# Performance work log

Hardware: AMD Instinct MI355X
Metric: run time of the kernel (lower is better)

Reference implementation:

```python
import jax, jax.numpy as jnp
import numpy as np

B, S, D_IN, D_OUT = 4, 2048, 1024, 1024

def setup_inputs() -> dict:
    key = jax.random.key(0)
    ks = jax.random.split(key, 6)
    s = 1.0 / np.sqrt(D_IN)
    return {
        "inputs": jax.random.normal(ks[0], (B, S, D_IN), dtype=jnp.float32),
        "Wq": jax.random.normal(ks[1], (D_IN, D_OUT), dtype=jnp.float32) * s,
        "Wk": jax.random.normal(ks[2], (D_IN, D_OUT), dtype=jnp.float32) * s,
        "Wv": jax.random.normal(ks[3], (D_IN, D_OUT), dtype=jnp.float32) * s,
        "Wo": jax.random.normal(ks[4], (D_OUT, D_OUT), dtype=jnp.float32) * (1.0 / np.sqrt(D_OUT)),
        "bo": jax.random.normal(ks[5], (D_OUT,), dtype=jnp.float32) * 0.01,
    }

def reference(inputs, Wq, Wk, Wv, Wo, bo):
    # QKV projections (no bias, matching qkv_bias=False)
    q = inputs @ Wq  # [B,S,D]
    k = inputs @ Wk
    v = inputs @ Wv
    # naive full attention: scores [B,S,S]
    scores = jnp.einsum('bqd,bkd->bqk', q, k) / jnp.sqrt(jnp.asarray(k.shape[-1], q.dtype))
    attn = jax.nn.softmax(scores, axis=-1)
    out = jnp.einsum('bqk,bkd->bqd', attn, v)
    return out @ Wo + bo
```

## Files before the change

kernel.cpp:

```cpp
#include <hip/hip_runtime.h>
#include <hip/hip_bf16.h>
#include <cstdint>

typedef __attribute__((ext_vector_type(8))) __bf16 bf16x8;
typedef __attribute__((ext_vector_type(4))) float  f32x4;

__device__ __forceinline__ unsigned short f2bf(float x) {
    union { float f; unsigned u; } v; v.f = x;
    unsigned r = v.u + 0x7fffu + ((v.u >> 16) & 1u);
    return (unsigned short)(r >> 16);
}
__device__ __forceinline__ unsigned pack2bf(float a, float b) {
    return (unsigned)f2bf(a) | ((unsigned)f2bf(b) << 16);
}

__device__ __forceinline__ void gld_lds16(const unsigned short* g, unsigned short* l) {
    __builtin_amdgcn_global_load_lds(
        (const __attribute__((address_space(1))) unsigned int*)g,
        (__attribute__((address_space(3))) unsigned int*)l,
        16, 0, 0);
}

__global__ void cvt_kernel(const float* __restrict__ in, unsigned short* __restrict__ out, int n4) {
    int i = blockIdx.x * blockDim.x + threadIdx.x;
    if (i < n4) {
        float4 f = ((const float4*)in)[i];
        ushort4 o;
        o.x = f2bf(f.x); o.y = f2bf(f.y); o.z = f2bf(f.z); o.w = f2bf(f.w);
        ((ushort4*)out)[i] = o;
    }
}

__global__ void wpack_kernel(const float* __restrict__ W, unsigned short* __restrict__ out) {
    int tid  = threadIdx.x;
    int lane = tid & 63;
    int chunk = blockIdx.x * 4 + (tid >> 6);
    int nt = chunk >> 5, k32 = chunk & 31;
    int r = lane & 15, q = lane >> 4;
    const float* src = W + (size_t)(k32*32 + q*8) * 1024 + nt*16 + r;
    unsigned o[4];
#pragma unroll
    for (int i = 0; i < 4; i++)
        o[i] = pack2bf(src[(size_t)(2*i) * 1024], src[(size_t)(2*i+1) * 1024]);
    *(uint4*)(out + (size_t)chunk * 512 + lane * 8) = make_uint4(o[0], o[1], o[2], o[3]);
}

__global__ void softmax_kernel(unsigned short* __restrict__ S) {
    const size_t row = blockIdx.x;
    unsigned short* p = S + row * 2048;
    const int tid = threadIdx.x;
    const int wave = tid >> 6, lane = tid & 63;

    uint4 raw = ((const uint4*)p)[tid];
    unsigned u[4] = {raw.x, raw.y, raw.z, raw.w};
    float x[8];
#pragma unroll
    for (int i = 0; i < 4; i++) {
        x[2*i]   = __uint_as_float(u[i] << 16);
        x[2*i+1] = __uint_as_float(u[i] & 0xffff0000u);
    }
    float m = x[0];
#pragma unroll
    for (int i = 1; i < 8; i++) m = fmaxf(m, x[i]);
#pragma unroll
    for (int off = 32; off >= 1; off >>= 1) m = fmaxf(m, __shfl_xor(m, off, 64));
    __shared__ float sm[4], ss[4];
    if (lane == 0) sm[wave] = m;
    __syncthreads();
    m = fmaxf(fmaxf(sm[0], sm[1]), fmaxf(sm[2], sm[3]));

    float e[8], s = 0.f;
#pragma unroll
    for (int i = 0; i < 8; i++) { e[i] = __expf(x[i] - m); s += e[i]; }
#pragma unroll
    for (int off = 32; off >= 1; off >>= 1) s += __shfl_xor(s, off, 64);
    if (lane == 0) ss[wave] = s;
    __syncthreads();
    s = ss[0] + ss[1] + ss[2] + ss[3];
    float inv = 1.0f / s;

    unsigned o[4];
#pragma unroll
    for (int i = 0; i < 4; i++)
        o[i] = pack2bf(e[2*i] * inv, e[2*i+1] * inv);
    ((uint4*)p)[tid] = make_uint4(o[0], o[1], o[2], o[3]);
}

template<int EPI>
__global__ __launch_bounds__(512, 2)
void gemm8p(const unsigned short* __restrict__ A, const unsigned short* __restrict__ Bpk,
            void* __restrict__ C, unsigned short* __restrict__ Ck, unsigned short* __restrict__ Cv,
            int lda, int ldc, int KS, int ns, float scale,
            long long sA, long long sB, long long sC)
{
    __shared__ __align__(16) char smem[131072];

    const int tid  = threadIdx.x;
    const int lane = tid & 63;
    const int wave = tid >> 6;
    const int bz = blockIdx.z;
    A   += (size_t)bz * sA;
    Bpk += (size_t)bz * sB;

    const int gx = gridDim.x;
    int lin = blockIdx.y * gx + blockIdx.x;
    int cpx = (gx * gridDim.y) >> 3;
    int swz = (lin & 7) * cpx + (lin >> 3);
    const int bm = (swz / gx) * 256;
    const int bn = (swz % gx) * 256;

    const int wm = (wave & 1) * 128;
    const int wn = (wave >> 1) * 64;
    const int ln15 = lane & 15;
    const int quad = lane >> 4;
    const int fko = (quad ^ ((ln15 >> 1) & 3)) * 8;

    const int srow = tid >> 2;
    const int scol = ((tid & 3) ^ ((tid >> 3) & 3)) * 8;
    const unsigned short* paU = A + (size_t)(bm + srow) * lda + scol;
    const unsigned short* paL = A + (size_t)(bm + 128 + srow) * lda + scol;
    const unsigned short* pb0 = Bpk + (size_t)((bn >> 4) + (tid >> 6)) * KS * 512 + lane * 8;
    const long long pbstep = (long long)8 * KS * 512;

    f32x4 acc[8][4];
#pragma unroll
    for (int i = 0; i < 8; i++)
#pragma unroll
        for (int j = 0; j < 4; j++) acc[i][j] = (f32x4){0.f, 0.f, 0.f, 0.f};

    auto stageA = [&](int buf, int t, int k) {
        char* d = smem + buf * 32768 + k * 16384 + tid * 16;
        const unsigned short* s = paU + t * 64 + k * 32;
        gld_lds16(s, (unsigned short*)d);
        gld_lds16(paL + t * 64 + k * 32, (unsigned short*)(d + 8192));
    };
    auto stageB = [&](int buf, int t, int k) {
        char* d = smem + 65536 + buf * 32768 + k * 16384 + (tid >> 6) * 1024 + lane * 16;
        const unsigned short* s = pb0 + (size_t)(2 * t + k) * 512;
        gld_lds16(s, (unsigned short*)d);
        gld_lds16(s + pbstep, (unsigned short*)(d + 8192));
    };
    auto phase = [&](int buf, int k, int mh) {
        const unsigned short* Ar = (const unsigned short*)(smem + buf * 32768 + k * 16384);
        const unsigned short* Br = (const unsigned short*)(smem + 65536 + buf * 32768 + k * 16384);
        bf16x8 af[4], bf[4];
#pragma unroll
        for (int i = 0; i < 4; i++)
            af[i] = *(const bf16x8*)&Ar[(wm + mh * 64 + i * 16 + ln15) * 32 + fko];
#pragma unroll
        for (int j = 0; j < 4; j++)
            bf[j] = *(const bf16x8*)&Br[((wn >> 4) + j) * 512 + lane * 8];
        __builtin_amdgcn_s_setprio(1);
#pragma unroll
        for (int i = 0; i < 4; i++)
#pragma unroll
            for (int j = 0; j < 4; j++)
                acc[mh * 4 + i][j] = __builtin_amdgcn_mfma_f32_16x16x32_bf16(
                    af[i], bf[j], acc[mh * 4 + i][j], 0, 0, 0);
        __builtin_amdgcn_s_setprio(0);
    };

#define SB  __builtin_amdgcn_sched_barrier(0)
#define FEN asm volatile("" ::: "memory")
    stageB(0, 0, 0); stageA(0, 0, 0); stageB(0, 0, 1); stageA(0, 0, 1); SB;

    for (int t = 0; t < ns; ++t) {
        const int buf = t & 1, nb = buf ^ 1;
        const int tn = (t + 1 < ns) ? t + 1 : 0;
        asm volatile("s_waitcnt vmcnt(4)" ::: "memory");
        __builtin_amdgcn_s_barrier(); FEN;
        stageB(nb, tn, 0); SB;
        phase(buf, 0, 0);
        __builtin_amdgcn_s_barrier(); FEN;
        stageA(nb, tn, 0); SB;
        phase(buf, 0, 1);
        asm volatile("s_waitcnt vmcnt(4)" ::: "memory");
        __builtin_amdgcn_s_barrier(); FEN;
        stageB(nb, tn, 1); SB;
        phase(buf, 1, 0);
        __builtin_amdgcn_s_barrier(); FEN;
        stageA(nb, tn, 1); SB;
        phase(buf, 1, 1);
    }
#undef SB
#undef FEN

    if (EPI == 1) {
        __syncthreads();
        float* ep = (float*)(smem + wave * 4352);
        unsigned short* Co = (unsigned short*)C + (size_t)bz * sC;
#pragma unroll
        for (int i = 0; i < 8; i++) {
#pragma unroll
            for (int j = 0; j < 4; j++)
#pragma unroll
                for (int r = 0; r < 4; r++)
                    ep[(quad*4 + r) * 68 + j*16 + ln15] = acc[i][j][r] * scale;
            __builtin_amdgcn_s_waitcnt(0);
#pragma unroll
            for (int pp = 0; pp < 2; pp++) {
                int lrow = pp*8 + (lane >> 3);
                int col0 = (lane & 7) * 8;
                float4 lo = *(const float4*)&ep[lrow * 68 + col0];
                float4 hi = *(const float4*)&ep[lrow * 68 + col0 + 4];
                uint4 o;
                o.x = pack2bf(lo.x, lo.y); o.y = pack2bf(lo.z, lo.w);
                o.z = pack2bf(hi.x, hi.y); o.w = pack2bf(hi.z, hi.w);
                *(uint4*)&Co[(size_t)(bm + wm + i*16 + lrow) * ldc + bn + wn + col0] = o;
            }
            __builtin_amdgcn_s_waitcnt(0);
        }
    } else {
        __syncthreads();
        float* ep = (float*)(smem + wave * 8704);
        const int region = bn >> 10;
#pragma unroll
        for (int g = 0; g < 4; g++) {
#pragma unroll
            for (int ii = 0; ii < 2; ii++) {
                int i = g*2 + ii;
#pragma unroll
                for (int j = 0; j < 4; j++)
#pragma unroll
                    for (int r = 0; r < 4; r++)
                        ep[(ii*16 + quad*4 + r) * 68 + j*16 + ln15] = acc[i][j][r] * scale;
            }
            __builtin_amdgcn_s_waitcnt(0);
            const int mrow0 = bm + wm + g*32;
            if (region == 0) {
                unsigned short* Q = (unsigned short*)C;
#pragma unroll
                for (int pp = 0; pp < 4; pp++) {
                    int lrow = pp*8 + (lane >> 3);
                    int col0 = (lane & 7) * 8;
                    float4 lo = *(const float4*)&ep[lrow * 68 + col0];
                    float4 hi = *(const float4*)&ep[lrow * 68 + col0 + 4];
                    uint4 o;
                    o.x = pack2bf(lo.x, lo.y); o.y = pack2bf(lo.z, lo.w);
                    o.z = pack2bf(hi.x, hi.y); o.w = pack2bf(hi.z, hi.w);
                    *(uint4*)&Q[(size_t)(mrow0 + lrow) * ldc + bn + wn + col0] = o;
                }
            } else if (region == 1) {
#pragma unroll
                for (int mt = 0; mt < 2; mt++)
#pragma unroll
                    for (int c = 0; c < 2; c++) {
                        float4 f0 = *(const float4*)&ep[(mt*16 + ln15) * 68 + c*32 + quad*8];
                        float4 f1 = *(const float4*)&ep[(mt*16 + ln15) * 68 + c*32 + quad*8 + 4];
                        uint4 o;
                        o.x = pack2bf(f0.x, f0.y); o.y = pack2bf(f0.z, f0.w);
                        o.z = pack2bf(f1.x, f1.y); o.w = pack2bf(f1.z, f1.w);
                        int cid = ((mrow0 + mt*16) >> 4) * 32 + ((bn - 1024 + wn + c*32) >> 5);
                        *(uint4*)(Ck + (size_t)cid * 512 + lane * 8) = o;
                    }
            } else {
                int s32 = mrow0 >> 5;
#pragma unroll
                for (int dt = 0; dt < 4; dt++) {
                    float v[8];
#pragma unroll
                    for (int e = 0; e < 8; e++)
                        v[e] = ep[(quad*8 + e) * 68 + dt*16 + ln15];
                    uint4 o;
                    o.x = pack2bf(v[0], v[1]); o.y = pack2bf(v[2], v[3]);
                    o.z = pack2bf(v[4], v[5]); o.w = pack2bf(v[6], v[7]);
                    int cid = (((bn - 2048 + wn) >> 4) + dt) * 256 + s32;
                    *(uint4*)(Cv + (size_t)cid * 512 + lane * 8) = o;
                }
            }
            __builtin_amdgcn_s_waitcnt(0);
        }
    }
}

template<int EPI>
__global__ __launch_bounds__(512, 2)
void gemm_pk(const unsigned short* __restrict__ A, const unsigned short* __restrict__ Bpk,
             void* __restrict__ C, unsigned short* __restrict__ Ck, unsigned short* __restrict__ Cv,
             const float* __restrict__ bias,
             int lda, int ldc, int KS, int ns, float scale,
             long long sA, long long sB, long long sC)
{
    __shared__ __align__(16) char smem[98304];

    const int tid  = threadIdx.x;
    const int lane = tid & 63;
    const int wave = tid >> 6;
    const int bz = blockIdx.z;
    A   += (size_t)bz * sA;
    Bpk += (size_t)bz * sB;

    const int gx = gridDim.x;
    int lin = blockIdx.y * gx + blockIdx.x;
    int cpx = (gx * gridDim.y) >> 3;
    int swz = (lin & 7) * cpx + (lin >> 3);
    const int bm = (swz / gx) * 256;
    const int bn = (swz % gx) * 128;

    const int srow = tid >> 2;
    const int scol = ((tid & 3) ^ ((tid >> 3) & 3)) * 8;
    const unsigned short* pa0 = A + (size_t)(bm + srow) * lda + scol;
    const unsigned short* pa1 = pa0 + 32;
    const unsigned short* pa2 = A + (size_t)(bm + 128 + srow) * lda + scol;
    const unsigned short* pa3 = pa2 + 32;

    const int wm = (wave & 3) * 64;
    const int wn = (wave >> 2) * 64;
    const int ln15 = lane & 15;
    const int quad = lane >> 4;
    const int fko = (quad ^ ((ln15 >> 1) & 3)) * 8;
    const int rbase = (wm >> 7) * 4096 + (wm & 127) * 32;
    const int ldsoff = tid * 16;

    const unsigned short* pb[4];
#pragma unroll
    for (int j = 0; j < 4; j++)
        pb[j] = Bpk + (size_t)(((bn + wn + j*16) >> 4) * KS) * 512 + lane * 8;

    f32x4 acc[4][4];
#pragma unroll
    for (int i = 0; i < 4; i++)
#pragma unroll
        for (int j = 0; j < 4; j++) acc[i][j] = (f32x4){0.f, 0.f, 0.f, 0.f};

    auto dma = [&](int buf) {
        char* base = smem + buf * 32768;
        gld_lds16(pa0, (unsigned short*)(base + ldsoff));
        gld_lds16(pa2, (unsigned short*)(base + 8192  + ldsoff));
        gld_lds16(pa1, (unsigned short*)(base + 16384 + ldsoff));
        gld_lds16(pa3, (unsigned short*)(base + 24576 + ldsoff));
        pa0 += 64; pa1 += 64; pa2 += 64; pa3 += 64;
    };
    auto loadB = [&](bf16x8* br) {
#pragma unroll
        for (int j = 0; j < 4; j++) {
            br[j]     = *(const bf16x8*)(pb[j]);
            br[4 + j] = *(const bf16x8*)(pb[j] + 512);
            pb[j] += 1024;
        }
    };
    auto phase = [&](const unsigned short* As, int t, const bf16x8* br) {
        bf16x8 af[4];
#pragma unroll
        for (int i = 0; i < 4; i++)
            af[i] = *(const bf16x8*)&As[t*8192 + rbase + i*512 + ln15*32 + fko];
        __builtin_amdgcn_s_setprio(1);
#pragma unroll
        for (int i = 0; i < 4; i++)
#pragma unroll
            for (int j = 0; j < 4; j++)
                acc[i][j] = __builtin_amdgcn_mfma_f32_16x16x32_bf16(
                    af[i], br[t*4 + j], acc[i][j], 0, 0, 0);
        __builtin_amdgcn_s_setprio(0);
    };

#define SB __builtin_amdgcn_sched_barrier(0)
    bf16x8 b0[8], b1[8];
    SB; dma(0); SB; loadB(b0); SB; dma(1); SB;

    int p = 0;
    for (int it = 0; it < ns; it += 2) {
        const unsigned short* As0 = (const unsigned short*)(smem + p * 32768);
        int p1 = p + 1; if (p1 >= 3) p1 -= 3;
        int q0 = p + 2; if (q0 >= 3) q0 -= 3;
        const unsigned short* As1 = (const unsigned short*)(smem + p1 * 32768);
        const bool more = (it + 2 < ns);

        asm volatile("s_waitcnt vmcnt(12)" ::: "memory");
        SB; __builtin_amdgcn_s_barrier(); SB;
        loadB(b1); SB;
        phase(As0, 0, b0);
        __builtin_amdgcn_s_barrier(); SB;
        if (more) { dma(q0); SB; }
        phase(As0, 1, b0);

        if (more) { asm volatile("s_waitcnt vmcnt(12)" ::: "memory"); }
        else      { asm volatile("s_waitcnt vmcnt(8)"  ::: "memory"); }
        SB; __builtin_amdgcn_s_barrier(); SB;
        if (more) { loadB(b0); SB; }
        phase(As1, 0, b1);
        __builtin_amdgcn_s_barrier(); SB;
        if (it + 3 < ns) { dma(p); SB; }
        phase(As1, 1, b1);

        p = q0;
    }
#undef SB

    if (EPI == 0) {
        float bval[4];
#pragma unroll
        for (int j = 0; j < 4; j++) bval[j] = bias[bn + wn + j*16 + ln15];
        float* Co = (float*)C + (size_t)bz * sC;
#pragma unroll
        for (int i = 0; i < 4; i++) {
            int r0 = bm + wm + i*16 + quad*4;
#pragma unroll
            for (int j = 0; j < 4; j++) {
                int c = bn + wn + j*16 + ln15;
#pragma unroll
                for (int r = 0; r < 4; r++)
                    Co[(size_t)(r0 + r) * ldc + c] = acc[i][j][r] * scale + bval[j];
            }
        }
    } else if (EPI == 1) {
        __syncthreads();
        float* ep = (float*)(smem + wave * 4352);
        unsigned short* Co = (unsigned short*)C + (size_t)bz * sC;
#pragma unroll
        for (int i = 0; i < 4; i++) {
#pragma unroll
            for (int j = 0; j < 4; j++)
#pragma unroll
                for (int r = 0; r < 4; r++)
                    ep[(quad*4 + r) * 68 + j*16 + ln15] = acc[i][j][r] * scale;
            __builtin_amdgcn_s_waitcnt(0);
#pragma unroll
            for (int pp = 0; pp < 2; pp++) {
                int lrow = pp*8 + (lane >> 3);
                int col0 = (lane & 7) * 8;
                float4 lo = *(const float4*)&ep[lrow * 68 + col0];
                float4 hi = *(const float4*)&ep[lrow * 68 + col0 + 4];
                uint4 o;
                o.x = pack2bf(lo.x, lo.y); o.y = pack2bf(lo.z, lo.w);
                o.z = pack2bf(hi.x, hi.y); o.w = pack2bf(hi.z, hi.w);
                *(uint4*)&Co[(size_t)(bm + wm + i*16 + lrow) * ldc + bn + wn + col0] = o;
            }
            __builtin_amdgcn_s_waitcnt(0);
        }
    }
}

extern "C" void kernel_launch(void* const* d_in, const int* in_sizes, int n_in,
                              void* d_out, int out_size, void* d_ws, size_t ws_size,
                              hipStream_t stream) {
    const float* X  = (const float*)d_in[0];
    const float* Wq = (const float*)d_in[1];
    const float* Wk = (const float*)d_in[2];
    const float* Wv = (const float*)d_in[3];
    const float* Wo = (const float*)d_in[4];
    const float* bo = (const float*)d_in[5];
    float* out = (float*)d_out;

    size_t off = 0;
    auto alloc = [&](size_t bytes) {
        void* p = (char*)d_ws + off;
        off += (bytes + 255) & ~(size_t)255;
        return p;
    };
    unsigned short* Xbf  = (unsigned short*)alloc(8192ull * 1024 * 2);
    unsigned short* Wpk  = (unsigned short*)alloc(192ull * 32 * 512 * 2);
    unsigned short* Wopk = (unsigned short*)alloc(64ull * 32 * 512 * 2);
    unsigned short* Qrm  = (unsigned short*)alloc(8192ull * 1024 * 2);
    unsigned short* Kpk  = (unsigned short*)alloc(512ull * 32 * 512 * 2);
    unsigned short* Vpk  = (unsigned short*)alloc(64ull * 256 * 512 * 2);
    unsigned short* Sc   = (unsigned short*)alloc(4ull * 2048 * 2048 * 2);
    unsigned short* AO   = Xbf;

    cvt_kernel<<<(8192*1024/4 + 255)/256, 256, 0, stream>>>(X, Xbf, 8192*1024/4);
    wpack_kernel<<<512, 256, 0, stream>>>(Wq, Wpk);
    wpack_kernel<<<512, 256, 0, stream>>>(Wk, Wpk + 64*32*512);
    wpack_kernel<<<512, 256, 0, stream>>>(Wv, Wpk + 128*32*512);
    wpack_kernel<<<512, 256, 0, stream>>>(Wo, Wopk);

    gemm8p<2><<<dim3(3072/256, 8192/256, 1), 512, 0, stream>>>(
        Xbf, Wpk, Qrm, Kpk, Vpk, 1024, 1024, 32, 16, 1.0f, 0, 0, 0);

    gemm8p<1><<<dim3(2048/256, 2048/256, 4), 512, 0, stream>>>(
        Qrm, Kpk, Sc, nullptr, nullptr, 1024, 2048, 32, 16, 0.03125f,
        2048ll*1024, 128ll*32*512, 2048ll*2048);

    softmax_kernel<<<8192, 256, 0, stream>>>(Sc);

    gemm_pk<1><<<dim3(1024/128, 2048/256, 4), 512, 0, stream>>>(
        Sc, Vpk, AO, nullptr, nullptr, nullptr, 2048, 1024, 256, 32, 1.0f,
        2048ll*2048, 64ll*512, 2048ll*1024);

    gemm_pk<0><<<dim3(1024/128, 8192/256, 1), 512, 0, stream>>>(
        AO, Wopk, out, nullptr, nullptr, bo, 1024, 1024, 32, 16, 1.0f, 0, 0, 0);

    (void)n_in; (void)in_sizes; (void)out_size; (void)ws_size;
}
```

Measured before the change: 284.4 us.

## Reorder GEMM main loop to issue LDS reads before global prefetch with explicit waits

Splits the per-phase work into separate LDS fragment reads and an MFMA block. Each quarter-iteration now issues its LDS reads first, then the next tile's global-to-LDS loads, and only then waits on lgkmcnt(0) before the MFMAs. The vmcnt waits move to the end of each k-half, and a wait plus barrier is added after the prologue. The aim is to overlap LDS latency with global-load issue and keep MFMA issue dense. The cost is twice as many workgroup barriers per iteration and a rigid schedule pinned by sched_barrier.

```diff
diff --git a/kernel.cpp b/kernel.cpp
--- a/kernel.cpp
+++ b/kernel.cpp
@@ -140,50 +140,52 @@
         gld_lds16(s, (unsigned short*)d);
         gld_lds16(s + pbstep, (unsigned short*)(d + 8192));
     };
-    auto phase = [&](int buf, int k, int mh) {
+    auto dsread = [&](int buf, int k, int mh, bf16x8* af, bf16x8* bfr) {
         const unsigned short* Ar = (const unsigned short*)(smem + buf * 32768 + k * 16384);
         const unsigned short* Br = (const unsigned short*)(smem + 65536 + buf * 32768 + k * 16384);
-        bf16x8 af[4], bf[4];
 #pragma unroll
         for (int i = 0; i < 4; i++)
             af[i] = *(const bf16x8*)&Ar[(wm + mh * 64 + i * 16 + ln15) * 32 + fko];
 #pragma unroll
         for (int j = 0; j < 4; j++)
-            bf[j] = *(const bf16x8*)&Br[((wn >> 4) + j) * 512 + lane * 8];
+            bfr[j] = *(const bf16x8*)&Br[((wn >> 4) + j) * 512 + lane * 8];
+    };
+    auto mfma16 = [&](int mh, const bf16x8* af, const bf16x8* bfr) {
         __builtin_amdgcn_s_setprio(1);
 #pragma unroll
         for (int i = 0; i < 4; i++)
 #pragma unroll
             for (int j = 0; j < 4; j++)
                 acc[mh * 4 + i][j] = __builtin_amdgcn_mfma_f32_16x16x32_bf16(
-                    af[i], bf[j], acc[mh * 4 + i][j], 0, 0, 0);
+                    af[i], bfr[j], acc[mh * 4 + i][j], 0, 0, 0);
         __builtin_amdgcn_s_setprio(0);
     };
 
-#define SB  __builtin_amdgcn_sched_barrier(0)
-#define FEN asm volatile("" ::: "memory")
+#define SB    __builtin_amdgcn_sched_barrier(0)
+#define BAR   __builtin_amdgcn_s_barrier()
+#define LGKM0 asm volatile("s_waitcnt lgkmcnt(0)" ::: "memory")
+#define VM4   asm volatile("s_waitcnt vmcnt(4)" ::: "memory")
+
     stageB(0, 0, 0); stageA(0, 0, 0); stageB(0, 0, 1); stageA(0, 0, 1); SB;
-
+    VM4; SB; BAR; SB;
+
+    bf16x8 af[4], bfr[4];
     for (int t = 0; t < ns; ++t) {
         const int buf = t & 1, nb = buf ^ 1;
         const int tn = (t + 1 < ns) ? t + 1 : 0;
-        asm volatile("s_waitcnt vmcnt(4)" ::: "memory");
-        __builtin_amdgcn_s_barrier(); FEN;
-        stageB(nb, tn, 0); SB;
-        phase(buf, 0, 0);
-        __builtin_amdgcn_s_barrier(); FEN;
-        stageA(nb, tn, 0); SB;
-        phase(buf, 0, 1);
-        asm volatile("s_waitcnt vmcnt(4)" ::: "memory");
-        __builtin_amdgcn_s_barrier(); FEN;
-        stageB(nb, tn, 1); SB;
-        phase(buf, 1, 0);
-        __builtin_amdgcn_s_barrier(); FEN;
-        stageA(nb, tn, 1); SB;
-        phase(buf, 1, 1);
+        dsread(buf, 0, 0, af, bfr); SB; stageB(nb, tn, 0); SB; BAR; SB;
+        LGKM0; SB; mfma16(0, af, bfr); SB; BAR; SB;
+        dsread(buf, 0, 1, af, bfr); SB; stageA(nb, tn, 0); SB; BAR; SB;
+        LGKM0; SB; mfma16(1, af, bfr); SB; VM4; SB; BAR; SB;
+        dsread(buf, 1, 0, af, bfr); SB; stageB(nb, tn, 1); SB; BAR; SB;
+        LGKM0; SB; mfma16(0, af, bfr); SB; BAR; SB;
+        dsread(buf, 1, 1, af, bfr); SB; stageA(nb, tn, 1); SB; BAR; SB;
+        LGKM0; SB; mfma16(1, af, bfr); SB; VM4; SB; BAR; SB;
     }
 #undef SB
-#undef FEN
+#undef BAR
+#undef LGKM0
+#undef VM4
 
     if (EPI == 1) {
         __syncthreads();
```

Result: no change. 287.3 us (+1.0%).
